# Kernel optimization log

Hardware: AMD Instinct MI355X
Metric: run time of the kernel (lower is better)

Reference implementation:

```python
import jax, jax.numpy as jnp
import numpy as np


def setup_inputs() -> dict:
    key = jax.random.key(0)
    kq, kk, kv = jax.random.split(key, 3)
    B, H, S, D = 2, 16, 2048, 128
    return {
        "q": jax.random.normal(kq, (B, H, S, D), dtype=jnp.float32),
        "k": jax.random.normal(kk, (B, H, S, D), dtype=jnp.float32),
        "v": jax.random.normal(kv, (B, H, S, D), dtype=jnp.float32),
    }


def reference(q, k, v):
    # scaled dot-product attention with causal mask (dropout in eval mode -> identity)
    d_k = k.shape[-1]
    scale = 1.0 / jnp.sqrt(jnp.asarray(d_k, dtype=q.dtype))
    # [B,H,Sq,Skv]
    attn = jnp.einsum("bhqd,bhkd->bhqk", q, k) * scale
    Sq = q.shape[-2]
    causal = jnp.triu(jnp.ones((Sq, Sq), dtype=bool), k=1)  # True above diagonal -> masked
    attn = jnp.where(causal, -jnp.inf, attn)
    attn = jax.nn.softmax(attn, axis=-1)
    return jnp.einsum("bhqk,bhkd->bhqd", attn, v)
```

## Files before the change

kernel.cpp:

```cpp
#include <hip/hip_runtime.h>

#define SQ 2048
#define DH 128
#define KVB 64
#define BHN 32
#define ELEMS ((size_t)BHN * SQ * DH)

typedef __bf16 bf16x8 __attribute__((ext_vector_type(8)));
typedef float f32x16 __attribute__((ext_vector_type(16)));
typedef unsigned uint2v __attribute__((ext_vector_type(2)));

__device__ __forceinline__ f32x16 mfma32(bf16x8 a, bf16x8 b, f32x16 c){
  return __builtin_amdgcn_mfma_f32_32x32x16_bf16(a, b, c, 0, 0, 0);
}

#define EXP2 __builtin_amdgcn_exp2f
#define GLD16(g, l) __builtin_amdgcn_global_load_lds( \
    (const __attribute__((address_space(1))) void*)(g), \
    (__attribute__((address_space(3))) void*)(l), 16, 0, 0)
#define VMCNT0 asm volatile("s_waitcnt vmcnt(0)" ::: "memory")
#define VMCNT4 asm volatile("s_waitcnt vmcnt(4)" ::: "memory")
#define VMCNT8 asm volatile("s_waitcnt vmcnt(8)" ::: "memory")
#define BARRIER asm volatile("s_barrier" ::: "memory")

__device__ __forceinline__ unsigned short f2bf(float f){
  unsigned u = __builtin_bit_cast(unsigned, f);
  u += 0x7fffu + ((u >> 16) & 1u);
  return (unsigned short)(u >> 16);
}
__device__ __forceinline__ unsigned packbf(float a, float b){
  return (unsigned)f2bf(a) | ((unsigned)f2bf(b) << 16);
}
__device__ __forceinline__ unsigned cvtpk(float a, float b){
  unsigned w;
  asm("v_cvt_pk_bf16_f32 %0, %1, %2" : "=v"(w) : "v"(a), "v"(b));
  return w;
}

#if __has_builtin(__builtin_amdgcn_permlane32_swap)
__device__ __forceinline__ void swap32p(unsigned a, unsigned b, unsigned &x, unsigned &y){
  uint2v r = __builtin_amdgcn_permlane32_swap(a, b, false, false);
  x = r[0]; y = r[1];
}
#else
__device__ __forceinline__ void swap32p(unsigned a, unsigned b, unsigned &x, unsigned &y){
  x = a; y = b;
  asm volatile("" : "+v"(x), "+v"(y));
  asm("v_permlane32_swap_b32 %0, %1" : "+v"(x), "+v"(y));
}
#endif
__device__ __forceinline__ float halfmax(float t){
  unsigned u = __builtin_bit_cast(unsigned, t), x, y;
  swap32p(u, u, x, y);
  return fmaxf(__builtin_bit_cast(float, x), __builtin_bit_cast(float, y));
}
__device__ __forceinline__ float halfadd(float t){
  unsigned u = __builtin_bit_cast(unsigned, t), x, y;
  swap32p(u, u, x, y);
  return __builtin_bit_cast(float, x) + __builtin_bit_cast(float, y);
}

__device__ __forceinline__ void swap32(unsigned a, unsigned b, bool h, unsigned &x, unsigned &y){
  unsigned sb = __shfl_xor(b, 32);
  unsigned sa = __shfl_xor(a, 32);
  x = h ? sb : a;
  y = h ? b : sa;
}

__device__ __forceinline__ bf16x8 mkfrag(unsigned w0, unsigned w1, unsigned w2, unsigned w3){
  uint4 t; t.x = w0; t.y = w1; t.z = w2; t.w = w3;
  return __builtin_bit_cast(bf16x8, t);
}

__global__ __launch_bounds__(256, 4)
void convkvt(const float* __restrict__ K, const float* __restrict__ V,
             unsigned short* __restrict__ Kb, unsigned short* __restrict__ Vt){
  if (blockIdx.x < 1024){
    const size_t g = (size_t)blockIdx.x * 256 + threadIdx.x;
    #pragma unroll
    for (int i = 0; i < 4; ++i){
      size_t e = (g + (size_t)i * 262144) * 8;
      float4 a = *(const float4*)(K + e);
      float4 b = *(const float4*)(K + e + 4);
      uint4 o;
      o.x = packbf(a.x, a.y); o.y = packbf(a.z, a.w);
      o.z = packbf(b.x, b.y); o.w = packbf(b.z, b.w);
      *(uint4*)(Kb + e) = o;
    }
  } else {
    __shared__ unsigned short T[64][65];
    const int bidx = blockIdx.x - 1024;
    const int dt = bidx & 1;
    const int kt = (bidx >> 1) & 31;
    const int bh = bidx >> 6;
    const float* src = V + (size_t)bh*SQ*DH + (size_t)kt*64*DH + dt*64;
    unsigned short* dst = Vt + (size_t)bh*DH*SQ + (size_t)dt*64*SQ + kt*64;
    const int t = threadIdx.x;
    const int c4 = (t & 15) * 4;
    const int r0 = t >> 4;
    #pragma unroll
    for (int i = 0; i < 4; ++i){
      int r = r0 + i*16;
      float4 f = *(const float4*)(src + (size_t)r*DH + c4);
      T[r][c4+0] = f2bf(f.x); T[r][c4+1] = f2bf(f.y);
      T[r][c4+2] = f2bf(f.z); T[r][c4+3] = f2bf(f.w);
    }
    __syncthreads();
    #pragma unroll
    for (int i = 0; i < 4; ++i){
      int d = r0 + i*16;
      ushort4 w;
      w.x = T[c4+0][d]; w.y = T[c4+1][d]; w.z = T[c4+2][d]; w.w = T[c4+3][d];
      *(ushort4*)(dst + (size_t)d*SQ + c4) = w;
    }
  }
}

__global__ __launch_bounds__(512, 2)
void attn_fwd_gl(const float* __restrict__ Q,
                 const unsigned short* __restrict__ Kbg,
                 const unsigned short* __restrict__ Vtg,
                 float* __restrict__ O)
{
  __shared__ __align__(16) unsigned char smem[131072];
  float* SF = (float*)smem;

  const int tid  = threadIdx.x;
  const int lane = tid & 63;
  const int wid  = tid >> 6;
  const int rg   = wid & 3;
  const int par  = wid >> 2;
  const int col  = lane & 31;
  const int hi   = lane >> 5;

  const int b   = blockIdx.x;
  const int xcd = b & 7;
  const int seq = b >> 3;
  const int bh4 = seq & 3;
  const int j   = seq >> 2;
  const int bh  = xcd + 8*bh4;

  const size_t base = (size_t)bh * SQ * DH;
  const float* Qg = Q + base;
  const unsigned short* Kb = Kbg + base;
  const unsigned short* Vt = Vtg + base;
  float* Og = O + base;

  const float SC = 0.08838834764831845f * 1.4426950408889634f;

  const unsigned short* ksrc[2];
  const unsigned short* vsrc[2];
  int kdst[2], vdst[2];
  #pragma unroll
  for (int i = 0; i < 2; ++i){
    int c = i*512 + tid;
    int r = c >> 4, dc = c & 15;
    ksrc[i] = Kb + (size_t)r*DH + ((dc ^ (r & 7)) * 8);
    kdst[i] = c * 16;
    int d = c >> 3, f = c & 7;
    vsrc[i] = Vt + (size_t)d*SQ + ((f ^ ((d >> 1) & 7)) * 8);
    vdst[i] = 16384 + c * 16;
  }

  auto LOADT = [&](int kvb, int bsel){
    const int bboff = bsel * 32768;
    #pragma unroll
    for (int i = 0; i < 2; ++i){
      GLD16(ksrc[i] + (size_t)kvb * DH, &smem[bboff + kdst[i]]);
      GLD16(vsrc[i] + kvb,              &smem[bboff + vdst[i]]);
    }
  };

  #pragma unroll 1
  for (int ph = 0; ph < 2; ++ph){
    const int qt = ph ? j : (15 - j);
    const int nt = 2*qt + 2;
    const int Q0 = qt*128 + rg*32;
    const int qg = Q0 + col;

    bf16x8 qf[8];
    #pragma unroll
    for (int dc = 0; dc < 8; ++dc){
      const float* src = Qg + (size_t)qg*DH + dc*16 + hi*8;
      float4 f0 = *(const float4*)(src);
      float4 f1 = *(const float4*)(src + 4);
      uint4 tq;
      tq.x = packbf(f0.x*SC, f0.y*SC); tq.y = packbf(f0.z*SC, f0.w*SC);
      tq.z = packbf(f1.x*SC, f1.y*SC); tq.w = packbf(f1.z*SC, f1.w*SC);
      qf[dc] = __builtin_bit_cast(bf16x8, tq);
    }

    f32x16 o0 = {}, o1 = {}, o2 = {}, o3 = {};
    float m = -1e30f, lsum = 0.f;

    LOADT(0, 0);
    if (nt > 1) LOADT(KVB, 1);
    if (nt > 2) LOADT(2*KVB, 2);
    if (nt > 2){ VMCNT8; } else { VMCNT4; }
    BARRIER;

    #pragma unroll 1
    for (int t = 0; t < nt; ++t){
      const int kvb = t * KVB;
      const int bboff = (t & 3) * 32768;
      const int myk = kvb + par*32;

      if (t + 3 < nt) LOADT(kvb + 3*KVB, (t + 3) & 3);

      if (myk <= Q0 + 31){
        f32x16 s0 = {};
        const int krow = par*32 + col;
        #pragma unroll
        for (int dc = 0; dc < 8; ++dc){
          uint4 rk = *(const uint4*)&smem[bboff + krow*256 + ((dc*32 + hi*16) ^ ((krow & 7) << 4))];
          s0 = mfma32(__builtin_bit_cast(bf16x8, rk), qf[dc], s0);
        }

        if (myk + 31 > Q0){
          #pragma unroll
          for (int r = 0; r < 16; ++r){
            int kl = (r & 3) + 8*(r >> 2) + 4*hi;
            if (myk + kl > qg) s0[r] = -1e30f;
          }
        }

        float p0 = fmaxf(s0[0],  s0[1]),  p1 = fmaxf(s0[2],  s0[3]);
        float p2 = fmaxf(s0[4],  s0[5]),  p3 = fmaxf(s0[6],  s0[7]);
        float p4 = fmaxf(s0[8],  s0[9]),  p5 = fmaxf(s0[10], s0[11]);
        float p6 = fmaxf(s0[12], s0[13]), p7 = fmaxf(s0[14], s0[15]);
        float q0v = fmaxf(p0, p1), q1v = fmaxf(p2, p3);
        float q2v = fmaxf(p4, p5), q3v = fmaxf(p6, p7);
        float tmax = halfmax(fmaxf(fmaxf(q0v, q1v), fmaxf(q2v, q3v)));
        if (!__all(tmax <= m + 8.0f)){
          float mnew  = fmaxf(m, tmax);
          float alpha = EXP2(m - mnew);
          m = mnew;
          lsum *= alpha;
          o0 *= alpha; o1 *= alpha; o2 *= alpha; o3 *= alpha;
        }

        float e0  = EXP2(s0[0]  - m), e1  = EXP2(s0[1]  - m);
        float e2  = EXP2(s0[2]  - m), e3  = EXP2(s0[3]  - m);
        float e4  = EXP2(s0[4]  - m), e5  = EXP2(s0[5]  - m);
        float e6  = EXP2(s0[6]  - m), e7  = EXP2(s0[7]  - m);
        float e8  = EXP2(s0[8]  - m), e9  = EXP2(s0[9]  - m);
        float e10 = EXP2(s0[10] - m), e11 = EXP2(s0[11] - m);
        float e12 = EXP2(s0[12] - m), e13 = EXP2(s0[13] - m);
        float e14 = EXP2(s0[14] - m), e15 = EXP2(s0[15] - m);
        lsum += (((e0+e1)+(e2+e3)) + ((e4+e5)+(e6+e7)))
              + (((e8+e9)+(e10+e11)) + ((e12+e13)+(e14+e15)));

        unsigned ua0 = cvtpk(e0,  e1),  ua1 = cvtpk(e2,  e3);
        unsigned ua2 = cvtpk(e4,  e5),  ua3 = cvtpk(e6,  e7);
        unsigned ua4 = cvtpk(e8,  e9),  ua5 = cvtpk(e10, e11);
        unsigned ua6 = cvtpk(e12, e13), ua7 = cvtpk(e14, e15);
        unsigned w0, w1, w2, w3;
        bf16x8 pf[2];
        swap32p(ua0, ua2, w0, w2); swap32p(ua1, ua3, w1, w3); pf[0] = mkfrag(w0,w1,w2,w3);
        swap32p(ua4, ua6, w0, w2); swap32p(ua5, ua7, w1, w3); pf[1] = mkfrag(w0,w1,w2,w3);

        #pragma unroll
        for (int cc = 0; cc < 2; ++cc){
          #pragma unroll
          for (int db = 0; db < 4; ++db){
            int rowd = db*32 + col;
            uint4 rv = *(const uint4*)&smem[bboff + 16384 + rowd*128 + ((par*64 + cc*32 + hi*16) ^ (((rowd >> 1) & 7) << 4))];
            f32x16& oo = (db==0)?o0:(db==1)?o1:(db==2)?o2:o3;
            oo = mfma32(__builtin_bit_cast(bf16x8, rv), pf[cc], oo);
          }
        }
      }

      if (t + 1 < nt){
        const int rem = nt - 2 - t;
        if (rem >= 2){ VMCNT8; } else if (rem == 1){ VMCNT4; } else { VMCNT0; }
      }
      BARRIER;
    }

    lsum = halfadd(lsum);

    float a0 = 1.f, a1 = 0.f, inv = 0.f;
    #pragma unroll 1
    for (int round = 0; round < 2; ++round){
      const f32x16& pa = round ? o2 : o0;
      const f32x16& pb = round ? o3 : o1;
      if (par == 1){
        #pragma unroll
        for (int i2 = 0; i2 < 16; ++i2){
          SF[rg*2048 + i2*64 + lane]      = pa[i2];
          SF[rg*2048 + (16+i2)*64 + lane] = pb[i2];
        }
        if (round == 0){
          SF[8192 + rg*64 + lane] = m;
          SF[8448 + rg*64 + lane] = lsum;
        }
      }
      __syncthreads();
      if (par == 0){
        if (round == 0){
          float m1 = SF[8192 + rg*64 + lane];
          float l1 = SF[8448 + rg*64 + lane];
          float ms = fmaxf(m, m1);
          a0 = EXP2(m - ms);
          a1 = EXP2(m1 - ms);
          float ls = lsum*a0 + l1*a1;
          inv = 1.0f / ls;
        }
        #pragma unroll
        for (int dbi = 0; dbi < 2; ++dbi){
          const f32x16& oo = round ? (dbi ? o3 : o2) : (dbi ? o1 : o0);
          const int db = round*2 + dbi;
          #pragma unroll
          for (int rg2 = 0; rg2 < 4; ++rg2){
            float4 w;
            w.x = (oo[rg2*4+0]*a0 + SF[rg*2048 + (dbi*16 + rg2*4+0)*64 + lane]*a1) * inv;
            w.y = (oo[rg2*4+1]*a0 + SF[rg*2048 + (dbi*16 + rg2*4+1)*64 + lane]*a1) * inv;
            w.z = (oo[rg2*4+2]*a0 + SF[rg*2048 + (dbi*16 + rg2*4+2)*64 + lane]*a1) * inv;
            w.w = (oo[rg2*4+3]*a0 + SF[rg*2048 + (dbi*16 + rg2*4+3)*64 + lane]*a1) * inv;
            *(float4*)(Og + (size_t)qg*DH + db*32 + rg2*8 + hi*4) = w;
          }
        }
      }
      __syncthreads();
    }
  }
}

__global__ __launch_bounds__(512, 2)
void attn_fwd_fb(const float* __restrict__ Q,
                 const float* __restrict__ Kf,
                 const float* __restrict__ Vf,
                 float* __restrict__ O)
{
  __shared__ __align__(16) unsigned char smem[65536];
  float* SF = (float*)smem;
  const int tid  = threadIdx.x;
  const int lane = tid & 63;
  const int wid  = tid >> 6;
  const int rg   = wid & 3;
  const int par  = wid >> 2;
  const int col  = lane & 31;
  const int hi   = lane >> 5;
  const int i4   = lane & 3;
  const int d0   = (lane >> 2)*8;
  const int b   = blockIdx.x;
  const int xcd = b & 7;
  const int seq = b >> 3;
  const int bh4 = seq & 3;
  const int j   = seq >> 2;
  const int bh  = xcd + 8*bh4;
  const size_t base = (size_t)bh * SQ * DH;
  const float* Qg = Q + base;
  const float* Kg = Kf + base;
  const float* Vg = Vf + base;
  float* Og = O + base;
  const float SC = 0.08838834764831845f * 1.4426950408889634f;
  float4 kr[4], vr[4];
  auto LOADT = [&](int kvb){
    #pragma unroll
    for (int i2 = 0; i2 < 2; ++i2){
      int c = i2*512 + tid, r = c >> 4, dc = c & 15;
      const float* src = Kg + (size_t)(kvb + r)*DH + dc*8;
      kr[2*i2]   = *(const float4*)(src);
      kr[2*i2+1] = *(const float4*)(src + 4);
    }
    #pragma unroll
    for (int it = 0; it < 2; ++it){
      int row = wid*8 + it*4 + i4;
      const float* src = Vg + (size_t)(kvb + row)*DH + d0;
      vr[2*it]   = *(const float4*)(src);
      vr[2*it+1] = *(const float4*)(src + 4);
    }
  };
  auto STORET = [&](int bsel){
    const int bboff = bsel * 32768;
    #pragma unroll
    for (int i2 = 0; i2 < 2; ++i2){
      int c = i2*512 + tid, r = c >> 4, dc = c & 15;
      uint4 kv;
      kv.x = packbf(kr[2*i2].x,   kr[2*i2].y);
      kv.y = packbf(kr[2*i2].z,   kr[2*i2].w);
      kv.z = packbf(kr[2*i2+1].x, kr[2*i2+1].y);
      kv.w = packbf(kr[2*i2+1].z, kr[2*i2+1].w);
      *(uint4*)&smem[bboff + r*256 + ((dc*16) ^ ((r & 7) << 4))] = kv;
    }
    #pragma unroll
    for (int it = 0; it < 2; ++it){
      int r0 = wid*8 + it*4;
      unsigned M0 = packbf(vr[2*it].x,   vr[2*it].y);
      unsigned M1 = packbf(vr[2*it].z,   vr[2*it].w);
      unsigned M2 = packbf(vr[2*it+1].x, vr[2*it+1].y);
      unsigned M3 = packbf(vr[2*it+1].z, vr[2*it+1].w);
      unsigned t0=__shfl_xor(M1,1), t1=__shfl_xor(M0,1), t2=__shfl_xor(M3,1), t3=__shfl_xor(M2,1);
      bool ob1 = i4 & 1;
      unsigned N0 = ob1 ? t0 : M0;
      unsigned N1 = ob1 ? M1 : t1;
      unsigned N2 = ob1 ? t2 : M2;
      unsigned N3 = ob1 ? M3 : t3;
      unsigned u0s=__shfl_xor(N2,2), u1s=__shfl_xor(N3,2), u2s=__shfl_xor(N0,2), u3s=__shfl_xor(N1,2);
      bool ob2 = i4 & 2;
      unsigned F0 = ob2 ? u0s : N0;
      unsigned F1 = ob2 ? u1s : N1;
      unsigned F2 = ob2 ? N2 : u2s;
      unsigned F3 = ob2 ? N3 : u3s;
      int d = d0 + 2*i4;
      unsigned lo0 = (F0 & 0xffffu) | (F1 << 16);
      unsigned lo1 = (F2 & 0xffffu) | (F3 << 16);
      unsigned hi0 = (F0 >> 16) | (F1 & 0xffff0000u);
      unsigned hi1 = (F2 >> 16) | (F3 & 0xffff0000u);
      int cb = r0*2;
      int sA = ((d >> 1) & 7) << 4;
      *(uint2*)&smem[bboff + 16384 + d*128     + (cb ^ sA)] = make_uint2(lo0, lo1);
      *(uint2*)&smem[bboff + 16384 + (d+1)*128 + (cb ^ sA)] = make_uint2(hi0, hi1);
    }
  };
  #pragma unroll 1
  for (int ph = 0; ph < 2; ++ph){
    const int qt = ph ? j : (15 - j);
    const int nt = 2*qt + 2;
    const int Q0 = qt*128 + rg*32;
    const int qg = Q0 + col;
    bf16x8 qf[8];
    #pragma unroll
    for (int dc = 0; dc < 8; ++dc){
      const float* src = Qg + (size_t)qg*DH + dc*16 + hi*8;
      float4 f0 = *(const float4*)(src);
      float4 f1 = *(const float4*)(src + 4);
      uint4 tq;
      tq.x = packbf(f0.x*SC, f0.y*SC); tq.y = packbf(f0.z*SC, f0.w*SC);
      tq.z = packbf(f1.x*SC, f1.y*SC); tq.w = packbf(f1.z*SC, f1.w*SC);
      qf[dc] = __builtin_bit_cast(bf16x8, tq);
    }
    f32x16 o0 = {}, o1 = {}, o2 = {}, o3 = {};
    float m = -1e30f, lsum = 0.f;
    LOADT(0);
    STORET(0);
    __syncthreads();
    #pragma unroll 1
    for (int t = 0; t < nt; ++t){
      const int kvb = t * KVB;
      const int bboff = (t & 1) * 32768;
      const int myk = kvb + par*32;
      if (t + 1 < nt) LOADT(kvb + KVB);
      if (myk <= Q0 + 31){
        f32x16 s0 = {};
        const int krow = par*32 + col;
        #pragma unroll
        for (int dc = 0; dc < 8; ++dc){
          uint4 rk = *(const uint4*)&smem[bboff + krow*256 + ((dc*32 + hi*16) ^ ((krow & 7) << 4))];
          s0 = mfma32(__builtin_bit_cast(bf16x8, rk), qf[dc], s0);
        }
        if (myk + 31 > Q0){
          #pragma unroll
          for (int r = 0; r < 16; ++r){
            int kl = (r & 3) + 8*(r >> 2) + 4*hi;
            if (myk + kl > qg) s0[r] = -1e30f;
          }
        }
        float tmax = -1e30f;
        #pragma unroll
        for (int r = 0; r < 16; ++r) tmax = fmaxf(tmax, s0[r]);
        tmax = fmaxf(tmax, __shfl_xor(tmax, 32));
        if (!__all(tmax <= m + 8.0f)){
          float mnew  = fmaxf(m, tmax);
          float alpha = EXP2(m - mnew);
          m = mnew;
          lsum *= alpha;
          o0 *= alpha; o1 *= alpha; o2 *= alpha; o3 *= alpha;
        }
        float ps = 0.f;
        #pragma unroll
        for (int r = 0; r < 16; ++r){ float e = EXP2(s0[r] - m); s0[r] = e; ps += e; }
        lsum += ps;
        unsigned ua0 = packbf(s0[0],  s0[1]),  ua1 = packbf(s0[2],  s0[3]);
        unsigned ua2 = packbf(s0[4],  s0[5]),  ua3 = packbf(s0[6],  s0[7]);
        unsigned ua4 = packbf(s0[8],  s0[9]),  ua5 = packbf(s0[10], s0[11]);
        unsigned ua6 = packbf(s0[12], s0[13]), ua7 = packbf(s0[14], s0[15]);
        bool h = (bool)hi;
        unsigned w0, w1, w2, w3;
        bf16x8 pf[2];
        swap32(ua0, ua2, h, w0, w2); swap32(ua1, ua3, h, w1, w3); pf[0] = mkfrag(w0,w1,w2,w3);
        swap32(ua4, ua6, h, w0, w2); swap32(ua5, ua7, h, w1, w3); pf[1] = mkfrag(w0,w1,w2,w3);
        #pragma unroll
        for (int cc = 0; cc < 2; ++cc){
          #pragma unroll
          for (int db = 0; db < 4; ++db){
            int rowd = db*32 + col;
            uint4 rv = *(const uint4*)&smem[bboff + 16384 + rowd*128 + ((par*64 + cc*32 + hi*16) ^ (((rowd >> 1) & 7) << 4))];
            f32x16& oo = (db==0)?o0:(db==1)?o1:(db==2)?o2:o3;
            oo = mfma32(__builtin_bit_cast(bf16x8, rv), pf[cc], oo);
          }
        }
      }
      if (t + 1 < nt) STORET((t + 1) & 1);
      __syncthreads();
    }
    lsum += __shfl_xor(lsum, 32);
    float a0 = 1.f, a1 = 0.f, inv = 0.f;
    #pragma unroll 1
    for (int round = 0; round < 2; ++round){
      const f32x16& pa = round ? o2 : o0;
      const f32x16& pb = round ? o3 : o1;
      if (par == 1){
        #pragma unroll
        for (int i2 = 0; i2 < 16; ++i2){
          SF[rg*2048 + i2*64 + lane]      = pa[i2];
          SF[rg*2048 + (16+i2)*64 + lane] = pb[i2];
        }
        if (round == 0){
          SF[8192 + rg*64 + lane] = m;
          SF[8448 + rg*64 + lane] = lsum;
        }
      }
      __syncthreads();
      if (par == 0){
        if (round == 0){
          float m1 = SF[8192 + rg*64 + lane];
          float l1 = SF[8448 + rg*64 + lane];
          float ms = fmaxf(m, m1);
          a0 = EXP2(m - ms);
          a1 = EXP2(m1 - ms);
          float ls = lsum*a0 + l1*a1;
          inv = 1.0f / ls;
        }
        #pragma unroll
        for (int dbi = 0; dbi < 2; ++dbi){
          const f32x16& oo = round ? (dbi ? o3 : o2) : (dbi ? o1 : o0);
          const int db = round*2 + dbi;
          #pragma unroll
          for (int rg2 = 0; rg2 < 4; ++rg2){
            float4 w;
            w.x = (oo[rg2*4+0]*a0 + SF[rg*2048 + (dbi*16 + rg2*4+0)*64 + lane]*a1) * inv;
            w.y = (oo[rg2*4+1]*a0 + SF[rg*2048 + (dbi*16 + rg2*4+1)*64 + lane]*a1) * inv;
            w.z = (oo[rg2*4+2]*a0 + SF[rg*2048 + (dbi*16 + rg2*4+2)*64 + lane]*a1) * inv;
            w.w = (oo[rg2*4+3]*a0 + SF[rg*2048 + (dbi*16 + rg2*4+3)*64 + lane]*a1) * inv;
            *(float4*)(Og + (size_t)qg*DH + db*32 + rg2*8 + hi*4) = w;
          }
        }
      }
      __syncthreads();
    }
  }
}

extern "C" void kernel_launch(void* const* d_in, const int* in_sizes, int n_in,
                              void* d_out, int out_size, void* d_ws, size_t ws_size,
                              hipStream_t stream) {
  const float* q = (const float*)d_in[0];
  const float* k = (const float*)d_in[1];
  const float* v = (const float*)d_in[2];
  float* out = (float*)d_out;

  const size_t need = 2 * ELEMS * sizeof(unsigned short);
  if (ws_size >= need){
    unsigned short* kb = (unsigned short*)d_ws;
    unsigned short* vt = kb + ELEMS;
    convkvt<<<3072, 256, 0, stream>>>(k, v, kb, vt);
    attn_fwd_gl<<<256, 512, 0, stream>>>(q, kb, vt, out);
  } else {
    attn_fwd_fb<<<256, 512, 0, stream>>>(q, k, v, out);
  }
}
```

Baseline: 85.37 us.

## Load K and V fragments directly into registers instead of staging through LDS

Replaces the 4-deep global_load_lds LDS ring buffer and its per-iteration barriers with per-wave direct global loads of K and V MFMA fragments into registers. K for the next tile is prefetched into a double-buffered register array, and V is loaded at the start of each step. This removes the LDS traffic and block-wide barrier synchronisation, and shrinks shared memory to the reduction scratch. In exchange it adds register pressure and exposes global-load latency, since V has no prefetch. It also uses uncoalesced strided 16-byte global reads, with each wave refetching data that was previously shared across waves.

```diff
diff --git a/kernel.cpp b/kernel.cpp
--- a/kernel.cpp
+++ b/kernel.cpp
@@ -15,13 +15,6 @@
 }
 
 #define EXP2 __builtin_amdgcn_exp2f
-#define GLD16(g, l) __builtin_amdgcn_global_load_lds( \
-    (const __attribute__((address_space(1))) void*)(g), \
-    (__attribute__((address_space(3))) void*)(l), 16, 0, 0)
-#define VMCNT0 asm volatile("s_waitcnt vmcnt(0)" ::: "memory")
-#define VMCNT4 asm volatile("s_waitcnt vmcnt(4)" ::: "memory")
-#define VMCNT8 asm volatile("s_waitcnt vmcnt(8)" ::: "memory")
-#define BARRIER asm volatile("s_barrier" ::: "memory")
 
 __device__ __forceinline__ unsigned short f2bf(float f){
   unsigned u = __builtin_bit_cast(unsigned, f);
@@ -117,13 +110,12 @@
 }
 
 __global__ __launch_bounds__(512, 2)
-void attn_fwd_gl(const float* __restrict__ Q,
-                 const unsigned short* __restrict__ Kbg,
-                 const unsigned short* __restrict__ Vtg,
-                 float* __restrict__ O)
+void attn_fwd_reg(const float* __restrict__ Q,
+                  const unsigned short* __restrict__ Kbg,
+                  const unsigned short* __restrict__ Vtg,
+                  float* __restrict__ O)
 {
-  __shared__ __align__(16) unsigned char smem[131072];
-  float* SF = (float*)smem;
+  __shared__ float SF[8704];
 
   const int tid  = threadIdx.x;
   const int lane = tid & 63;
@@ -148,28 +140,7 @@
 
   const float SC = 0.08838834764831845f * 1.4426950408889634f;
 
-  const unsigned short* ksrc[2];
-  const unsigned short* vsrc[2];
-  int kdst[2], vdst[2];
-  #pragma unroll
-  for (int i = 0; i < 2; ++i){
-    int c = i*512 + tid;
-    int r = c >> 4, dc = c & 15;
-    ksrc[i] = Kb + (size_t)r*DH + ((dc ^ (r & 7)) * 8);
-    kdst[i] = c * 16;
-    int d = c >> 3, f = c & 7;
-    vsrc[i] = Vt + (size_t)d*SQ + ((f ^ ((d >> 1) & 7)) * 8);
-    vdst[i] = 16384 + c * 16;
-  }
-
-  auto LOADT = [&](int kvb, int bsel){
-    const int bboff = bsel * 32768;
-    #pragma unroll
-    for (int i = 0; i < 2; ++i){
-      GLD16(ksrc[i] + (size_t)kvb * DH, &smem[bboff + kdst[i]]);
-      GLD16(vsrc[i] + kvb,              &smem[bboff + vdst[i]]);
-    }
-  };
+  const int krow_l = par*32 + col;
 
   #pragma unroll 1
   for (int ph = 0; ph < 2; ++ph){
@@ -193,34 +164,47 @@
     f32x16 o0 = {}, o1 = {}, o2 = {}, o3 = {};
     float m = -1e30f, lsum = 0.f;
 
-    LOADT(0, 0);
-    if (nt > 1) LOADT(KVB, 1);
-    if (nt > 2) LOADT(2*KVB, 2);
-    if (nt > 2){ VMCNT8; } else { VMCNT4; }
-    BARRIER;
-
-    #pragma unroll 1
-    for (int t = 0; t < nt; ++t){
+    uint4 kfA[8], kfB[8];
+
+    if (krow_l <= Q0 + 31){
+      const unsigned short* p = Kb + (size_t)krow_l*DH + hi*8;
+      #pragma unroll
+      for (int dc = 0; dc < 8; ++dc) kfA[dc] = *(const uint4*)(p + dc*16);
+    }
+
+    auto STEP = [&](int t, uint4 (&kcur)[8], uint4 (&knext)[8]){
       const int kvb = t * KVB;
-      const int bboff = (t & 3) * 32768;
-      const int myk = kvb + par*32;
-
-      if (t + 3 < nt) LOADT(kvb + 3*KVB, (t + 3) & 3);
-
-      if (myk <= Q0 + 31){
+      const int myk = kvb + krow_l;
+
+      if (t + 1 < nt && (kvb + KVB + krow_l) <= qg + (31 - col) + 0){
+      }
+      if (t + 1 < nt && (kvb + KVB + par*32) <= Q0 + 31){
+        const unsigned short* p = Kb + (size_t)(kvb + KVB + krow_l)*DH + hi*8;
+        #pragma unroll
+        for (int dc = 0; dc < 8; ++dc) knext[dc] = *(const uint4*)(p + dc*16);
+      }
+
+      if (kvb + par*32 <= Q0 + 31){
+        uint4 vfr[8];
+        #pragma unroll
+        for (int cc = 0; cc < 2; ++cc){
+          #pragma unroll
+          for (int db = 0; db < 4; ++db){
+            vfr[cc*4+db] = *(const uint4*)(Vt + (size_t)(db*32 + col)*SQ
+                                           + kvb + par*32 + cc*16 + hi*8);
+          }
+        }
+
         f32x16 s0 = {};
-        const int krow = par*32 + col;
-        #pragma unroll
-        for (int dc = 0; dc < 8; ++dc){
-          uint4 rk = *(const uint4*)&smem[bboff + krow*256 + ((dc*32 + hi*16) ^ ((krow & 7) << 4))];
-          s0 = mfma32(__builtin_bit_cast(bf16x8, rk), qf[dc], s0);
-        }
-
-        if (myk + 31 > Q0){
+        #pragma unroll
+        for (int dc = 0; dc < 8; ++dc)
+          s0 = mfma32(__builtin_bit_cast(bf16x8, kcur[dc]), qf[dc], s0);
+
+        if (myk - col + 31 > Q0){
           #pragma unroll
           for (int r = 0; r < 16; ++r){
             int kl = (r & 3) + 8*(r >> 2) + 4*hi;
-            if (myk + kl > qg) s0[r] = -1e30f;
+            if (kvb + par*32 + kl > qg) s0[r] = -1e30f;
           }
         }
 
@@ -228,9 +212,8 @@
         float p2 = fmaxf(s0[4],  s0[5]),  p3 = fmaxf(s0[6],  s0[7]);
         float p4 = fmaxf(s0[8],  s0[9]),  p5 = fmaxf(s0[10], s0[11]);
         float p6 = fmaxf(s0[12], s0[13]), p7 = fmaxf(s0[14], s0[15]);
-        float q0v = fmaxf(p0, p1), q1v = fmaxf(p2, p3);
-        float q2v = fmaxf(p4, p5), q3v = fmaxf(p6, p7);
-        float tmax = halfmax(fmaxf(fmaxf(q0v, q1v), fmaxf(q2v, q3v)));
+        float tmax = halfmax(fmaxf(fmaxf(fmaxf(p0,p1), fmaxf(p2,p3)),
+                                   fmaxf(fmaxf(p4,p5), fmaxf(p6,p7))));
         if (!__all(tmax <= m + 8.0f)){
           float mnew  = fmaxf(m, tmax);
           float alpha = EXP2(m - mnew);
@@ -263,19 +246,17 @@
         for (int cc = 0; cc < 2; ++cc){
           #pragma unroll
           for (int db = 0; db < 4; ++db){
-            int rowd = db*32 + col;
-            uint4 rv = *(const uint4*)&smem[bboff + 16384 + rowd*128 + ((par*64 + cc*32 + hi*16) ^ (((rowd >> 1) & 7) << 4))];
             f32x16& oo = (db==0)?o0:(db==1)?o1:(db==2)?o2:o3;
-            oo = mfma32(__builtin_bit_cast(bf16x8, rv), pf[cc], oo);
-          }
-        }
-      }
-
-      if (t + 1 < nt){
-        const int rem = nt - 2 - t;
-        if (rem >= 2){ VMCNT8; } else if (rem == 1){ VMCNT4; } else { VMCNT0; }
-      }
-      BARRIER;
+            oo = mfma32(__builtin_bit_cast(bf16x8, vfr[cc*4+db]), pf[cc], oo);
+          }
+        }
+      }
+    };
+
+    #pragma unroll 1
+    for (int t = 0; t < nt; t += 2){
+      STEP(t,     kfA, kfB);
+      STEP(t + 1, kfB, kfA);
     }
 
     lsum = halfadd(lsum);
@@ -557,7 +538,7 @@
     unsigned short* kb = (unsigned short*)d_ws;
     unsigned short* vt = kb + ELEMS;
     convkvt<<<3072, 256, 0, stream>>>(k, v, kb, vt);
-    attn_fwd_gl<<<256, 512, 0, stream>>>(q, kb, vt, out);
+    attn_fwd_reg<<<256, 512, 0, stream>>>(q, kb, vt, out);
   } else {
     attn_fwd_fb<<<256, 512, 0, stream>>>(q, k, v, out);
   }
```

New measurement: 154.3 us. 80.8% more time.
